# Kernel tuning notes

Hardware: AMD Instinct MI355X
Metric: run time of the kernel (lower is better)

Reference implementation:

```python
import jax, jax.numpy as jnp
import numpy as np

LN_EPS = 1e-6  # flax.linen.LayerNorm default

def _layernorm(x, scale, bias):
    mu = jnp.mean(x, axis=-1, keepdims=True)
    var = jnp.mean(jnp.square(x - mu), axis=-1, keepdims=True)
    return (x - mu) * jax.lax.rsqrt(var + LN_EPS) * scale + bias

def setup_inputs() -> dict:
    key = jax.random.key(0)
    ks = jax.random.split(key, 16)
    N, D = 65536, 512
    W = 1024  # hidden width for all 4 layers
    def init_w(k, fan_in, fan_out):
        # lecun_normal (flax Dense default kernel init)
        return jax.random.normal(k, (fan_in, fan_out), jnp.float32) / np.sqrt(fan_in)
    return {
        "descriptors": jax.random.normal(ks[0], (N, D), jnp.float32),
        "W0": init_w(ks[1], D, W),
        "b0": jnp.zeros((W,), jnp.float32),
        "W1": init_w(ks[2], W, W),
        "g1": jnp.ones((W,), jnp.float32),
        "be1": jnp.zeros((W,), jnp.float32),
        "W2": init_w(ks[3], W, W),
        "g2": jnp.ones((W,), jnp.float32),
        "be2": jnp.zeros((W,), jnp.float32),
        "W3": init_w(ks[4], W, W),
        "g3": jnp.ones((W,), jnp.float32),
        "be3": jnp.zeros((W,), jnp.float32),
        "Wout": init_w(ks[5], W, 1),
        "bout": jnp.zeros((1,), jnp.float32),
    }

def reference(descriptors, W0, b0, W1, g1, be1, W2, g2, be2, W3, g3, be3, Wout, bout):
    # layer 0: Dense (with bias) -> relu
    h = jax.nn.relu(descriptors @ W0 + b0)  # [N, 1024]
    # hidden layers: bias-free Dense -> LayerNorm -> relu
    for Wk, gk, bk in ((W1, g1, be1), (W2, g2, be2), (W3, g3, be3)):
        h = jax.nn.relu(_layernorm(h @ Wk, gk, bk))
    # output: Dense(1) with bias -> relu
    return jax.nn.relu(h @ Wout + bout)  # [N, 1]
```

## Files before the change

### kernel.cpp

```cpp
#include <hip/hip_runtime.h>

typedef _Float16 f16;
typedef _Float16 f16x8 __attribute__((ext_vector_type(8)));
typedef float f32x16 __attribute__((ext_vector_type(16)));

#define TM 128
#define TN 256
#define BK 64

__device__ __forceinline__ void async_cp16(const void* g, void* l) {
  __builtin_amdgcn_global_load_lds(
      (const __attribute__((address_space(1))) void*)g,
      (__attribute__((address_space(3))) void*)l, 16, 0, 0);
}

template <int LNA, int EPI>
__global__ __launch_bounds__(256, 2) void gemm_f16(
    const f16* __restrict__ Af16, const float* __restrict__ Af32,
    const f16* __restrict__ Bt, const float* __restrict__ bias,
    f16* __restrict__ C, int M, int N, int K) {
  __shared__ alignas(16) f16 sA[TM][BK];
  __shared__ alignas(16) f16 sB[TN][BK];
  const int tid = threadIdx.x;
  const int lane = tid & 63;
  const int wave = tid >> 6;

  int mt, nt;
  if (gridDim.x == 4 && gridDim.y == 512) {
    const int id = blockIdx.y * 4 + blockIdx.x;
    nt = (id >> 3) & 3;
    mt = (id & 7) * 64 + (id >> 5);
  } else {
    nt = blockIdx.x;
    mt = blockIdx.y;
  }
  const long long bm = (long long)mt * TM;
  const long long bn = (long long)nt * TN;

  const int wm = (wave & 1) * 64;
  const int wn = (wave >> 1) * 128;
  const int l31 = lane & 31;
  const int half = lane >> 5;

  const f16* const Abase = Af16 + bm * (long long)K;
  const float* const A32base = Af32 ? (Af32 + bm * (long long)K) : nullptr;
  const f16* const Bbase = Bt + bn * (long long)K;
  int aOff[4], bOff[8];
#pragma unroll
  for (int i = 0; i < 4; ++i) {
    const int chunk = wave * 256 + i * 64 + lane;
    const int ml = chunk >> 3;
    const int kc = (chunk & 7) ^ (ml & 7);
    aOff[i] = ml * K + kc * 8;
  }
#pragma unroll
  for (int i = 0; i < 8; ++i) {
    const int chunk = wave * 512 + i * 64 + lane;
    const int ml = chunk >> 3;
    const int kc = (chunk & 7) ^ (ml & 7);
    bOff[i] = ml * K + kc * 8;
  }

  f32x16 acc[2][4] = {};

  const int kIters = K / BK;
  for (int kt = 0; kt < kIters; ++kt) {
    const int k0 = kt * BK;
    if (LNA == 0) {
#pragma unroll
      for (int i = 0; i < 4; ++i)
        async_cp16(Abase + aOff[i] + k0, &sA[0][0] + (wave * 256 + i * 64) * 8);
    } else {
#pragma unroll
      for (int i = 0; i < 4; ++i) {
        float xv[8];
        *(float4*)(xv) = *(const float4*)(A32base + aOff[i] + k0);
        *(float4*)(xv + 4) = *(const float4*)(A32base + aOff[i] + k0 + 4);
        f16x8 o;
#pragma unroll
        for (int e = 0; e < 8; ++e) o[e] = (f16)xv[e];
        *(f16x8*)(&sA[0][0] + (wave * 256 + i * 64 + lane) * 8) = o;
      }
    }
#pragma unroll
    for (int i = 0; i < 8; ++i)
      async_cp16(Bbase + bOff[i] + k0, &sB[0][0] + (wave * 512 + i * 64) * 8);
    __syncthreads();

#pragma unroll
    for (int s = 0; s < 4; ++s) {
      const int csw = ((s * 2 + half) ^ (lane & 7)) * 8;
      f16x8 af[2], bf[4];
#pragma unroll
      for (int i = 0; i < 2; ++i) af[i] = *(const f16x8*)&sA[wm + i * 32 + l31][csw];
#pragma unroll
      for (int j = 0; j < 4; ++j) bf[j] = *(const f16x8*)&sB[wn + j * 32 + l31][csw];
#pragma unroll
      for (int i = 0; i < 2; ++i)
#pragma unroll
        for (int j = 0; j < 4; ++j)
          acc[i][j] = __builtin_amdgcn_mfma_f32_32x32x16_f16(af[i], bf[j],
                                                             acc[i][j], 0, 0, 0);
    }
    __syncthreads();
  }

#pragma unroll
  for (int i = 0; i < 2; ++i)
#pragma unroll
    for (int j = 0; j < 4; ++j) {
      const long long colg = bn + wn + j * 32 + l31;
      float bval = 0.f;
      if (EPI == 0) bval = bias[colg];
#pragma unroll
      for (int reg = 0; reg < 16; ++reg) {
        const long long rowg =
            bm + wm + i * 32 + (reg & 3) + 8 * (reg >> 2) + 4 * half;
        float v = acc[i][j][reg];
        if (EPI == 0) v = fmaxf(v + bval, 0.f);
        C[rowg * N + colg] = (f16)v;
      }
    }
}

__global__ __launch_bounds__(256) void ln_relu_kernel(
    const f16* __restrict__ Y, const float* __restrict__ g,
    const float* __restrict__ b, f16* __restrict__ H) {
  const int lane = threadIdx.x & 63;
  const int wave = threadIdx.x >> 6;
  const long long row = (long long)blockIdx.x * 4 + wave;
  const f16* y = Y + row * 1024;
  float x[16];
  float s1 = 0.f, s2 = 0.f;
#pragma unroll
  for (int p = 0; p < 2; ++p) {
    f16x8 v = *(const f16x8*)(y + p * 512 + lane * 8);
#pragma unroll
    for (int e = 0; e < 8; ++e) {
      const float f = (float)v[e];
      x[p * 8 + e] = f;
      s1 += f;
      s2 += f * f;
    }
  }
#pragma unroll
  for (int off = 32; off >= 1; off >>= 1) {
    s1 += __shfl_xor(s1, off);
    s2 += __shfl_xor(s2, off);
  }
  const float mean = s1 * (1.f / 1024.f);
  const float var = fmaxf(s2 * (1.f / 1024.f) - mean * mean, 0.f);
  const float inv = rsqrtf(var + 1e-6f);
  f16* h = H + row * 1024;
#pragma unroll
  for (int p = 0; p < 2; ++p) {
    f16x8 o;
#pragma unroll
    for (int e = 0; e < 8; ++e) {
      const int c = p * 512 + lane * 8 + e;
      const float v = (x[p * 8 + e] - mean) * inv * g[c] + b[c];
      o[e] = (f16)fmaxf(v, 0.f);
    }
    *(f16x8*)(h + p * 512 + lane * 8) = o;
  }
}

__global__ __launch_bounds__(256) void ln_relu_out_kernel(
    const f16* __restrict__ Y, const float* __restrict__ g,
    const float* __restrict__ b, const float* __restrict__ Wout,
    const float* __restrict__ bout, float* __restrict__ out) {
  const int lane = threadIdx.x & 63;
  const int wave = threadIdx.x >> 6;
  const long long row = (long long)blockIdx.x * 4 + wave;
  const f16* y = Y + row * 1024;
  float x[16];
  float s1 = 0.f, s2 = 0.f;
#pragma unroll
  for (int p = 0; p < 2; ++p) {
    f16x8 v = *(const f16x8*)(y + p * 512 + lane * 8);
#pragma unroll
    for (int e = 0; e < 8; ++e) {
      const float f = (float)v[e];
      x[p * 8 + e] = f;
      s1 += f;
      s2 += f * f;
    }
  }
#pragma unroll
  for (int off = 32; off >= 1; off >>= 1) {
    s1 += __shfl_xor(s1, off);
    s2 += __shfl_xor(s2, off);
  }
  const float mean = s1 * (1.f / 1024.f);
  const float var = fmaxf(s2 * (1.f / 1024.f) - mean * mean, 0.f);
  const float inv = rsqrtf(var + 1e-6f);
  float dot = 0.f;
#pragma unroll
  for (int p = 0; p < 2; ++p) {
#pragma unroll
    for (int e = 0; e < 8; ++e) {
      const int c = p * 512 + lane * 8 + e;
      const float v = fmaxf((x[p * 8 + e] - mean) * inv * g[c] + b[c], 0.f);
      dot += v * Wout[c];
    }
  }
#pragma unroll
  for (int off = 32; off >= 1; off >>= 1) dot += __shfl_xor(dot, off);
  if (lane == 0) out[row] = fmaxf(dot + bout[0], 0.f);
}

__global__ __launch_bounds__(256) void transpose_cvt_all(
    const float* __restrict__ W0, const float* __restrict__ W1,
    const float* __restrict__ W2, const float* __restrict__ W3,
    f16* __restrict__ Wt0, f16* __restrict__ Wt1, f16* __restrict__ Wt2,
    f16* __restrict__ Wt3) {
  const int z = blockIdx.z;
  const float* W = z == 0 ? W0 : (z == 1 ? W1 : (z == 2 ? W2 : W3));
  f16* Wt = z == 0 ? Wt0 : (z == 1 ? Wt1 : (z == 2 ? Wt2 : Wt3));
  const int K = z == 0 ? 512 : 1024;
  const int N = 1024;
  const int bk = blockIdx.y * 64;
  if (bk >= K) return;
  __shared__ float tile[64][65];
  const int bn = blockIdx.x * 64;
  const int tx = threadIdx.x & 63;
  const int ty = threadIdx.x >> 6;
#pragma unroll
  for (int i = 0; i < 64; i += 4)
    tile[ty + i][tx] = W[(long long)(bk + ty + i) * N + bn + tx];
  __syncthreads();
#pragma unroll
  for (int i = 0; i < 64; i += 4)
    Wt[(long long)(bn + ty + i) * K + bk + tx] = (f16)tile[tx][ty + i];
}

extern "C" void kernel_launch(void* const* d_in, const int* in_sizes, int n_in,
                              void* d_out, int out_size, void* d_ws, size_t ws_size,
                              hipStream_t stream) {
  const float* desc = (const float*)d_in[0];
  const float* W0 = (const float*)d_in[1];
  const float* b0 = (const float*)d_in[2];
  const float* W1 = (const float*)d_in[3];
  const float* g1 = (const float*)d_in[4];
  const float* be1 = (const float*)d_in[5];
  const float* W2 = (const float*)d_in[6];
  const float* g2 = (const float*)d_in[7];
  const float* be2 = (const float*)d_in[8];
  const float* W3 = (const float*)d_in[9];
  const float* g3 = (const float*)d_in[10];
  const float* be3 = (const float*)d_in[11];
  const float* Wout = (const float*)d_in[12];
  const float* bout = (const float*)d_in[13];
  float* out = (float*)d_out;

  const long long Nrows = 65536, D = 512, W = 1024;
  char* p = (char*)d_ws;
  f16* Wt0 = (f16*)p;   p += D * W * sizeof(f16);
  f16* Wt1 = (f16*)p;   p += W * W * sizeof(f16);
  f16* Wt2 = (f16*)p;   p += W * W * sizeof(f16);
  f16* Wt3 = (f16*)p;   p += W * W * sizeof(f16);
  f16* H = (f16*)p;     p += Nrows * W * sizeof(f16);
  f16* Y = (f16*)p;     p += Nrows * W * sizeof(f16);
  (void)ws_size; (void)in_sizes; (void)n_in; (void)out_size;

  transpose_cvt_all<<<dim3(16, 16, 4), 256, 0, stream>>>(W0, W1, W2, W3, Wt0,
                                                         Wt1, Wt2, Wt3);

  dim3 ggrid(W / TN, Nrows / TM);

  gemm_f16<2, 0><<<ggrid, 256, 0, stream>>>(nullptr, desc, Wt0, b0, H,
                                            (int)Nrows, (int)W, (int)D);

  gemm_f16<0, 1><<<ggrid, 256, 0, stream>>>(H, nullptr, Wt1, nullptr, Y,
                                            (int)Nrows, (int)W, (int)W);
  ln_relu_kernel<<<(int)(Nrows / 4), 256, 0, stream>>>(Y, g1, be1, H);

  gemm_f16<0, 1><<<ggrid, 256, 0, stream>>>(H, nullptr, Wt2, nullptr, Y,
                                            (int)Nrows, (int)W, (int)W);
  ln_relu_kernel<<<(int)(Nrows / 4), 256, 0, stream>>>(Y, g2, be2, H);

  gemm_f16<0, 1><<<ggrid, 256, 0, stream>>>(H, nullptr, Wt3, nullptr, Y,
                                            (int)Nrows, (int)W, (int)W);

  ln_relu_out_kernel<<<(int)(Nrows / 4), 256, 0, stream>>>(Y, g3, be3, Wout,
                                                           bout, out);
}
```

Measured before the change: 862.2 us.

## Fuse all layers into one persistent cooperative kernel with grid syncs

```diff
diff --git a/kernel.cpp b/kernel.cpp
--- a/kernel.cpp
+++ b/kernel.cpp
@@ -1,4 +1,7 @@
 #include <hip/hip_runtime.h>
+#include <hip/hip_cooperative_groups.h>
+
+namespace cg = cooperative_groups;
 
 typedef _Float16 f16;
 typedef _Float16 f16x8 __attribute__((ext_vector_type(8)));
@@ -13,6 +16,302 @@
       (const __attribute__((address_space(1))) void*)g,
       (__attribute__((address_space(3))) void*)l, 16, 0, 0);
 }
+
+
+template <int LNA, int EPI>
+__device__ __forceinline__ void gemm_tile_body(
+    f16 (&sA)[TM][BK], f16 (&sB)[TN][BK], const f16* __restrict__ Af16,
+    const float* __restrict__ Af32, const f16* __restrict__ Bt,
+    const float* __restrict__ bias, f16* __restrict__ C, int mt, int nt,
+    int N, int K) {
+  const int tid = threadIdx.x;
+  const int lane = tid & 63;
+  const int wave = tid >> 6;
+  const long long bm = (long long)mt * TM;
+  const long long bn = (long long)nt * TN;
+  const int wm = (wave & 1) * 64;
+  const int wn = (wave >> 1) * 128;
+  const int l31 = lane & 31;
+  const int half = lane >> 5;
+
+  const f16* const Abase = (LNA == 0) ? Af16 + bm * (long long)K : nullptr;
+  const float* const A32base = (LNA == 2) ? Af32 + bm * (long long)K : nullptr;
+  const f16* const Bbase = Bt + bn * (long long)K;
+  int aOff[4], bOff[8];
+#pragma unroll
+  for (int i = 0; i < 4; ++i) {
+    const int chunk = wave * 256 + i * 64 + lane;
+    const int ml = chunk >> 3;
+    const int kc = (chunk & 7) ^ (ml & 7);
+    aOff[i] = ml * K + kc * 8;
+  }
+#pragma unroll
+  for (int i = 0; i < 8; ++i) {
+    const int chunk = wave * 512 + i * 64 + lane;
+    const int ml = chunk >> 3;
+    const int kc = (chunk & 7) ^ (ml & 7);
+    bOff[i] = ml * K + kc * 8;
+  }
+
+  f32x16 acc[2][4] = {};
+
+  const int kIters = K / BK;
+  for (int kt = 0; kt < kIters; ++kt) {
+    const int k0 = kt * BK;
+    if (LNA == 0) {
+#pragma unroll
+      for (int i = 0; i < 4; ++i)
+        async_cp16(Abase + aOff[i] + k0, &sA[0][0] + (wave * 256 + i * 64) * 8);
+    } else {
+#pragma unroll
+      for (int i = 0; i < 4; ++i) {
+        float xv[8];
+        *(float4*)(xv) = *(const float4*)(A32base + aOff[i] + k0);
+        *(float4*)(xv + 4) = *(const float4*)(A32base + aOff[i] + k0 + 4);
+        f16x8 o;
+#pragma unroll
+        for (int e = 0; e < 8; ++e) o[e] = (f16)xv[e];
+        *(f16x8*)(&sA[0][0] + (wave * 256 + i * 64 + lane) * 8) = o;
+      }
+    }
+#pragma unroll
+    for (int i = 0; i < 8; ++i)
+      async_cp16(Bbase + bOff[i] + k0, &sB[0][0] + (wave * 512 + i * 64) * 8);
+    __syncthreads();
+
+#pragma unroll
+    for (int s = 0; s < 4; ++s) {
+      const int csw = ((s * 2 + half) ^ (lane & 7)) * 8;
+      f16x8 af[2], bf[4];
+#pragma unroll
+      for (int i = 0; i < 2; ++i) af[i] = *(const f16x8*)&sA[wm + i * 32 + l31][csw];
+#pragma unroll
+      for (int j = 0; j < 4; ++j) bf[j] = *(const f16x8*)&sB[wn + j * 32 + l31][csw];
+#pragma unroll
+      for (int i = 0; i < 2; ++i)
+#pragma unroll
+        for (int j = 0; j < 4; ++j)
+          acc[i][j] = __builtin_amdgcn_mfma_f32_32x32x16_f16(af[i], bf[j],
+                                                             acc[i][j], 0, 0, 0);
+    }
+    __syncthreads();
+  }
+
+#pragma unroll
+  for (int i = 0; i < 2; ++i)
+#pragma unroll
+    for (int j = 0; j < 4; ++j) {
+      const long long colg = bn + wn + j * 32 + l31;
+      float bval = 0.f;
+      if (EPI == 0) bval = bias[colg];
+#pragma unroll
+      for (int reg = 0; reg < 16; ++reg) {
+        const long long rowg =
+            bm + wm + i * 32 + (reg & 3) + 8 * (reg >> 2) + 4 * half;
+        float v = acc[i][j][reg];
+        if (EPI == 0) v = fmaxf(v + bval, 0.f);
+        C[rowg * N + colg] = (f16)v;
+      }
+    }
+}
+
+__device__ __forceinline__ void tile_remap(int id, int& mt, int& nt) {
+  nt = (id >> 3) & 3;
+  mt = (id & 7) * 64 + (id >> 5);
+}
+
+__device__ __forceinline__ void ln_row_body(const f16* __restrict__ y,
+                                            const float* __restrict__ g,
+                                            const float* __restrict__ b,
+                                            f16* __restrict__ h, int lane) {
+  float x[16];
+  float s1 = 0.f, s2 = 0.f;
+#pragma unroll
+  for (int p = 0; p < 2; ++p) {
+    f16x8 v = *(const f16x8*)(y + p * 512 + lane * 8);
+#pragma unroll
+    for (int e = 0; e < 8; ++e) {
+      const float f = (float)v[e];
+      x[p * 8 + e] = f;
+      s1 += f;
+      s2 += f * f;
+    }
+  }
+#pragma unroll
+  for (int off = 32; off >= 1; off >>= 1) {
+    s1 += __shfl_xor(s1, off);
+    s2 += __shfl_xor(s2, off);
+  }
+  const float mean = s1 * (1.f / 1024.f);
+  const float var = fmaxf(s2 * (1.f / 1024.f) - mean * mean, 0.f);
+  const float inv = rsqrtf(var + 1e-6f);
+#pragma unroll
+  for (int p = 0; p < 2; ++p) {
+    f16x8 o;
+#pragma unroll
+    for (int e = 0; e < 8; ++e) {
+      const int c = p * 512 + lane * 8 + e;
+      const float v = (x[p * 8 + e] - mean) * inv * g[c] + b[c];
+      o[e] = (f16)fmaxf(v, 0.f);
+    }
+    *(f16x8*)(h + p * 512 + lane * 8) = o;
+  }
+}
+
+__device__ __forceinline__ void ln_out_row_body(
+    const f16* __restrict__ y, const float* __restrict__ g,
+    const float* __restrict__ b, const float* __restrict__ Wout,
+    const float* __restrict__ bout, float* __restrict__ outp, int lane) {
+  float x[16];
+  float s1 = 0.f, s2 = 0.f;
+#pragma unroll
+  for (int p = 0; p < 2; ++p) {
+    f16x8 v = *(const f16x8*)(y + p * 512 + lane * 8);
+#pragma unroll
+    for (int e = 0; e < 8; ++e) {
+      const float f = (float)v[e];
+      x[p * 8 + e] = f;
+      s1 += f;
+      s2 += f * f;
+    }
+  }
+#pragma unroll
+  for (int off = 32; off >= 1; off >>= 1) {
+    s1 += __shfl_xor(s1, off);
+    s2 += __shfl_xor(s2, off);
+  }
+  const float mean = s1 * (1.f / 1024.f);
+  const float var = fmaxf(s2 * (1.f / 1024.f) - mean * mean, 0.f);
+  const float inv = rsqrtf(var + 1e-6f);
+  float dot = 0.f;
+#pragma unroll
+  for (int p = 0; p < 2; ++p) {
+#pragma unroll
+    for (int e = 0; e < 8; ++e) {
+      const int c = p * 512 + lane * 8 + e;
+      const float v = fmaxf((x[p * 8 + e] - mean) * inv * g[c] + b[c], 0.f);
+      dot += v * Wout[c];
+    }
+  }
+#pragma unroll
+  for (int off = 32; off >= 1; off >>= 1) dot += __shfl_xor(dot, off);
+  if (lane == 0) *outp = fmaxf(dot + bout[0], 0.f);
+}
+
+__device__ __forceinline__ void transpose_body(const float* __restrict__ W,
+                                               f16* __restrict__ Wt, int K,
+                                               int bx, int by,
+                                               float (&tile)[64][65]) {
+  const int bk = by * 64;
+  const int bn = bx * 64;
+  const int tx = threadIdx.x & 63;
+  const int ty = threadIdx.x >> 6;
+  const bool act = bk < K;
+  if (act) {
+#pragma unroll
+    for (int i = 0; i < 64; i += 4)
+      tile[ty + i][tx] = W[(long long)(bk + ty + i) * 1024 + bn + tx];
+  }
+  __syncthreads();
+  if (act) {
+#pragma unroll
+    for (int i = 0; i < 64; i += 4)
+      Wt[(long long)(bn + ty + i) * K + bk + tx] = (f16)tile[tx][ty + i];
+  }
+}
+
+
+union MegaSM {
+  struct {
+    alignas(16) f16 A[TM][BK];
+    alignas(16) f16 B[TN][BK];
+  } g;
+  float tr[64][65];
+};
+
+__global__ __launch_bounds__(256, 2) void fused_net(
+    const float* __restrict__ desc, const float* __restrict__ W0,
+    const float* __restrict__ b0, const float* __restrict__ W1,
+    const float* __restrict__ g1, const float* __restrict__ be1,
+    const float* __restrict__ W2, const float* __restrict__ g2,
+    const float* __restrict__ be2, const float* __restrict__ W3,
+    const float* __restrict__ g3, const float* __restrict__ be3,
+    const float* __restrict__ Wout, const float* __restrict__ bout,
+    f16* __restrict__ Wt0, f16* __restrict__ Wt1, f16* __restrict__ Wt2,
+    f16* __restrict__ Wt3, f16* __restrict__ H, f16* __restrict__ Y,
+    float* __restrict__ out) {
+  __shared__ MegaSM sm;
+  cg::grid_group grid = cg::this_grid();
+  const int bid = blockIdx.x;
+  const int lane = threadIdx.x & 63;
+  const int wave = threadIdx.x >> 6;
+
+  for (int t = bid; t < 1024; t += 512) {
+    const int z = t >> 8, rem = t & 255, by = rem >> 4, bx = rem & 15;
+    const float* Ws = z == 0 ? W0 : (z == 1 ? W1 : (z == 2 ? W2 : W3));
+    f16* Wd = z == 0 ? Wt0 : (z == 1 ? Wt1 : (z == 2 ? Wt2 : Wt3));
+    transpose_body(Ws, Wd, z == 0 ? 512 : 1024, bx, by, sm.tr);
+    __syncthreads();
+  }
+  __threadfence();
+  grid.sync();
+
+  for (int t = bid; t < 2048; t += 512) {
+    int mt, nt;
+    tile_remap(t, mt, nt);
+    gemm_tile_body<2, 0>(sm.g.A, sm.g.B, nullptr, desc, Wt0, b0, H, mt, nt,
+                         1024, 512);
+  }
+  __threadfence();
+  grid.sync();
+
+  for (int t = bid; t < 2048; t += 512) {
+    int mt, nt;
+    tile_remap(t, mt, nt);
+    gemm_tile_body<0, 1>(sm.g.A, sm.g.B, H, nullptr, Wt1, nullptr, Y, mt, nt,
+                         1024, 1024);
+  }
+  __threadfence();
+  grid.sync();
+
+  for (int rb = bid; rb < 16384; rb += 512) {
+    const long long row = (long long)rb * 4 + wave;
+    ln_row_body(Y + row * 1024, g1, be1, H + row * 1024, lane);
+  }
+  __threadfence();
+  grid.sync();
+
+  for (int t = bid; t < 2048; t += 512) {
+    int mt, nt;
+    tile_remap(t, mt, nt);
+    gemm_tile_body<0, 1>(sm.g.A, sm.g.B, H, nullptr, Wt2, nullptr, Y, mt, nt,
+                         1024, 1024);
+  }
+  __threadfence();
+  grid.sync();
+
+  for (int rb = bid; rb < 16384; rb += 512) {
+    const long long row = (long long)rb * 4 + wave;
+    ln_row_body(Y + row * 1024, g2, be2, H + row * 1024, lane);
+  }
+  __threadfence();
+  grid.sync();
+
+  for (int t = bid; t < 2048; t += 512) {
+    int mt, nt;
+    tile_remap(t, mt, nt);
+    gemm_tile_body<0, 1>(sm.g.A, sm.g.B, H, nullptr, Wt3, nullptr, Y, mt, nt,
+                         1024, 1024);
+  }
+  __threadfence();
+  grid.sync();
+
+  for (int rb = bid; rb < 16384; rb += 512) {
+    const long long row = (long long)rb * 4 + wave;
+    ln_out_row_body(Y + row * 1024, g3, be3, Wout, bout, out + row, lane);
+  }
+}
+
 
 template <int LNA, int EPI>
 __global__ __launch_bounds__(256, 2) void gemm_f16(
@@ -21,106 +320,15 @@
     f16* __restrict__ C, int M, int N, int K) {
   __shared__ alignas(16) f16 sA[TM][BK];
   __shared__ alignas(16) f16 sB[TN][BK];
-  const int tid = threadIdx.x;
-  const int lane = tid & 63;
-  const int wave = tid >> 6;
-
   int mt, nt;
   if (gridDim.x == 4 && gridDim.y == 512) {
     const int id = blockIdx.y * 4 + blockIdx.x;
-    nt = (id >> 3) & 3;
-    mt = (id & 7) * 64 + (id >> 5);
+    tile_remap(id, mt, nt);
   } else {
     nt = blockIdx.x;
     mt = blockIdx.y;
   }
-  const long long bm = (long long)mt * TM;
-  const long long bn = (long long)nt * TN;
-
-  const int wm = (wave & 1) * 64;
-  const int wn = (wave >> 1) * 128;
-  const int l31 = lane & 31;
-  const int half = lane >> 5;
-
-  const f16* const Abase = Af16 + bm * (long long)K;
-  const float* const A32base = Af32 ? (Af32 + bm * (long long)K) : nullptr;
-  const f16* const Bbase = Bt + bn * (long long)K;
-  int aOff[4], bOff[8];
-#pragma unroll
-  for (int i = 0; i < 4; ++i) {
-    const int chunk = wave * 256 + i * 64 + lane;
-    const int ml = chunk >> 3;
-    const int kc = (chunk & 7) ^ (ml & 7);
-    aOff[i] = ml * K + kc * 8;
-  }
-#pragma unroll
-  for (int i = 0; i < 8; ++i) {
-    const int chunk = wave * 512 + i * 64 + lane;
-    const int ml = chunk >> 3;
-    const int kc = (chunk & 7) ^ (ml & 7);
-    bOff[i] = ml * K + kc * 8;
-  }
-
-  f32x16 acc[2][4] = {};
-
-  const int kIters = K / BK;
-  for (int kt = 0; kt < kIters; ++kt) {
-    const int k0 = kt * BK;
-    if (LNA == 0) {
-#pragma unroll
-      for (int i = 0; i < 4; ++i)
-        async_cp16(Abase + aOff[i] + k0, &sA[0][0] + (wave * 256 + i * 64) * 8);
-    } else {
-#pragma unroll
-      for (int i = 0; i < 4; ++i) {
-        float xv[8];
-        *(float4*)(xv) = *(const float4*)(A32base + aOff[i] + k0);
-        *(float4*)(xv + 4) = *(const float4*)(A32base + aOff[i] + k0 + 4);
-        f16x8 o;
-#pragma unroll
-        for (int e = 0; e < 8; ++e) o[e] = (f16)xv[e];
-        *(f16x8*)(&sA[0][0] + (wave * 256 + i * 64 + lane) * 8) = o;
-      }
-    }
-#pragma unroll
-    for (int i = 0; i < 8; ++i)
-      async_cp16(Bbase + bOff[i] + k0, &sB[0][0] + (wave * 512 + i * 64) * 8);
-    __syncthreads();
-
-#pragma unroll
-    for (int s = 0; s < 4; ++s) {
-      const int csw = ((s * 2 + half) ^ (lane & 7)) * 8;
-      f16x8 af[2], bf[4];
-#pragma unroll
-      for (int i = 0; i < 2; ++i) af[i] = *(const f16x8*)&sA[wm + i * 32 + l31][csw];
-#pragma unroll
-      for (int j = 0; j < 4; ++j) bf[j] = *(const f16x8*)&sB[wn + j * 32 + l31][csw];
-#pragma unroll
-      for (int i = 0; i < 2; ++i)
-#pragma unroll
-        for (int j = 0; j < 4; ++j)
-          acc[i][j] = __builtin_amdgcn_mfma_f32_32x32x16_f16(af[i], bf[j],
-                                                             acc[i][j], 0, 0, 0);
-    }
-    __syncthreads();
-  }
-
-#pragma unroll
-  for (int i = 0; i < 2; ++i)
-#pragma unroll
-    for (int j = 0; j < 4; ++j) {
-      const long long colg = bn + wn + j * 32 + l31;
-      float bval = 0.f;
-      if (EPI == 0) bval = bias[colg];
-#pragma unroll
-      for (int reg = 0; reg < 16; ++reg) {
-        const long long rowg =
-            bm + wm + i * 32 + (reg & 3) + 8 * (reg >> 2) + 4 * half;
-        float v = acc[i][j][reg];
-        if (EPI == 0) v = fmaxf(v + bval, 0.f);
-        C[rowg * N + colg] = (f16)v;
-      }
-    }
+  gemm_tile_body<LNA, EPI>(sA, sB, Af16, Af32, Bt, bias, C, mt, nt, N, K);
 }
 
 __global__ __launch_bounds__(256) void ln_relu_kernel(
@@ -129,40 +337,7 @@
   const int lane = threadIdx.x & 63;
   const int wave = threadIdx.x >> 6;
   const long long row = (long long)blockIdx.x * 4 + wave;
-  const f16* y = Y + row * 1024;
-  float x[16];
-  float s1 = 0.f, s2 = 0.f;
-#pragma unroll
-  for (int p = 0; p < 2; ++p) {
-    f16x8 v = *(const f16x8*)(y + p * 512 + lane * 8);
-#pragma unroll
-    for (int e = 0; e < 8; ++e) {
-      const float f = (float)v[e];
-      x[p * 8 + e] = f;
-      s1 += f;
-      s2 += f * f;
-    }
-  }
-#pragma unroll
-  for (int off = 32; off >= 1; off >>= 1) {
-    s1 += __shfl_xor(s1, off);
-    s2 += __shfl_xor(s2, off);
-  }
-  const float mean = s1 * (1.f / 1024.f);
-  const float var = fmaxf(s2 * (1.f / 1024.f) - mean * mean, 0.f);
-  const float inv = rsqrtf(var + 1e-6f);
-  f16* h = H + row * 1024;
-#pragma unroll
-  for (int p = 0; p < 2; ++p) {
-    f16x8 o;
-#pragma unroll
-    for (int e = 0; e < 8; ++e) {
-      const int c = p * 512 + lane * 8 + e;
-      const float v = (x[p * 8 + e] - mean) * inv * g[c] + b[c];
-      o[e] = (f16)fmaxf(v, 0.f);
-    }
-    *(f16x8*)(h + p * 512 + lane * 8) = o;
-  }
+  ln_row_body(Y + row * 1024, g, b, H + row * 1024, lane);
 }
 
 __global__ __launch_bounds__(256) void ln_relu_out_kernel(
@@ -172,41 +347,7 @@
   const int lane = threadIdx.x & 63;
   const int wave = threadIdx.x >> 6;
   const long long row = (long long)blockIdx.x * 4 + wave;
-  const f16* y = Y + row * 1024;
-  float x[16];
-  float s1 = 0.f, s2 = 0.f;
-#pragma unroll
-  for (int p = 0; p < 2; ++p) {
-    f16x8 v = *(const f16x8*)(y + p * 512 + lane * 8);
-#pragma unroll
-    for (int e = 0; e < 8; ++e) {
-      const float f = (float)v[e];
-      x[p * 8 + e] = f;
-      s1 += f;
-      s2 += f * f;
-    }
-  }
-#pragma unroll
-  for (int off = 32; off >= 1; off >>= 1) {
-    s1 += __shfl_xor(s1, off);
-    s2 += __shfl_xor(s2, off);
-  }
-  const float mean = s1 * (1.f / 1024.f);
-  const float var = fmaxf(s2 * (1.f / 1024.f) - mean * mean, 0.f);
-  const float inv = rsqrtf(var + 1e-6f);
-  float dot = 0.f;
-#pragma unroll
-  for (int p = 0; p < 2; ++p) {
-#pragma unroll
-    for (int e = 0; e < 8; ++e) {
-      const int c = p * 512 + lane * 8 + e;
-      const float v = fmaxf((x[p * 8 + e] - mean) * inv * g[c] + b[c], 0.f);
-      dot += v * Wout[c];
-    }
-  }
-#pragma unroll
-  for (int off = 32; off >= 1; off >>= 1) dot += __shfl_xor(dot, off);
-  if (lane == 0) out[row] = fmaxf(dot + bout[0], 0.f);
+  ln_out_row_body(Y + row * 1024, g, b, Wout, bout, out + row, lane);
 }
 
 __global__ __launch_bounds__(256) void transpose_cvt_all(
@@ -214,24 +355,11 @@
     const float* __restrict__ W2, const float* __restrict__ W3,
     f16* __restrict__ Wt0, f16* __restrict__ Wt1, f16* __restrict__ Wt2,
     f16* __restrict__ Wt3) {
+  __shared__ float tile[64][65];
   const int z = blockIdx.z;
   const float* W = z == 0 ? W0 : (z == 1 ? W1 : (z == 2 ? W2 : W3));
   f16* Wt = z == 0 ? Wt0 : (z == 1 ? Wt1 : (z == 2 ? Wt2 : Wt3));
-  const int K = z == 0 ? 512 : 1024;
-  const int N = 1024;
-  const int bk = blockIdx.y * 64;
-  if (bk >= K) return;
-  __shared__ float tile[64][65];
-  const int bn = blockIdx.x * 64;
-  const int tx = threadIdx.x & 63;
-  const int ty = threadIdx.x >> 6;
-#pragma unroll
-  for (int i = 0; i < 64; i += 4)
-    tile[ty + i][tx] = W[(long long)(bk + ty + i) * N + bn + tx];
-  __syncthreads();
-#pragma unroll
-  for (int i = 0; i < 64; i += 4)
-    Wt[(long long)(bn + ty + i) * K + bk + tx] = (f16)tile[tx][ty + i];
+  transpose_body(W, Wt, z == 0 ? 512 : 1024, blockIdx.x, blockIdx.y, tile);
 }
 
 extern "C" void kernel_launch(void* const* d_in, const int* in_sizes, int n_in,
@@ -263,25 +391,27 @@
   f16* Y = (f16*)p;     p += Nrows * W * sizeof(f16);
   (void)ws_size; (void)in_sizes; (void)n_in; (void)out_size;
 
+  void* kargs[] = {&desc, &W0, &b0, &W1, &g1, &be1, &W2, &g2, &be2,
+                   &W3, &g3, &be3, &Wout, &bout, &Wt0, &Wt1, &Wt2, &Wt3,
+                   &H, &Y, &out};
+  const hipError_t err = hipLaunchCooperativeKernel(
+      reinterpret_cast<void*>(fused_net), dim3(512), dim3(256), kargs, 0,
+      stream);
+  if (err == hipSuccess) return;
+
   transpose_cvt_all<<<dim3(16, 16, 4), 256, 0, stream>>>(W0, W1, W2, W3, Wt0,
                                                          Wt1, Wt2, Wt3);
-
   dim3 ggrid(W / TN, Nrows / TM);
-
   gemm_f16<2, 0><<<ggrid, 256, 0, stream>>>(nullptr, desc, Wt0, b0, H,
                                             (int)Nrows, (int)W, (int)D);
-
   gemm_f16<0, 1><<<ggrid, 256, 0, stream>>>(H, nullptr, Wt1, nullptr, Y,
                                             (int)Nrows, (int)W, (int)W);
   ln_relu_kernel<<<(int)(Nrows / 4), 256, 0, stream>>>(Y, g1, be1, H);
-
   gemm_f16<0, 1><<<ggrid, 256, 0, stream>>>(H, nullptr, Wt2, nullptr, Y,
                                             (int)Nrows, (int)W, (int)W);
   ln_relu_kernel<<<(int)(Nrows / 4), 256, 0, stream>>>(Y, g2, be2, H);
-
   gemm_f16<0, 1><<<ggrid, 256, 0, stream>>>(H, nullptr, Wt3, nullptr, Y,
                                             (int)Nrows, (int)W, (int)W);
-
   ln_relu_out_kernel<<<(int)(Nrows / 4), 256, 0, stream>>>(Y, g3, be3, Wout,
                                                            bout, out);
 }
```

Result: slower. 1.753 ms (+103.3%).
